# Performance work log

Measured on AMD Instinct MI355X. Metric: run time of the kernel, lower is better.

## Reference

```python
import jax, jax.numpy as jnp
import numpy as np
from jax import lax

LATENT = 64
NUM_EMB = 512
BETA = 0.25
DN = ('NCHW', 'OIHW', 'NCHW')


def conv(x, w, b, stride, pad):
    y = lax.conv_general_dilated(x, w, (stride, stride), [(pad, pad), (pad, pad)],
                                 dimension_numbers=DN)
    return y + b[None, :, None, None]


def tconv(x, w, b, stride, pad, opad):
    # torch ConvTranspose2d(k=3, stride, padding=pad, output_padding=opad)
    # == dilated conv with lhs_dilation=stride, padding (k-1-pad, k-1-pad+opad),
    #    spatially-flipped kernel. w is stored OIHW (out, in, kh, kw).
    k = w.shape[2]
    lo, hi = k - 1 - pad, k - 1 - pad + opad
    y = lax.conv_general_dilated(x, w[:, :, ::-1, ::-1], (1, 1), [(lo, hi), (lo, hi)],
                                 lhs_dilation=(stride, stride), dimension_numbers=DN)
    return y + b[None, :, None, None]


def vector_quantize(z, codebook):
    # z: (B, D, H, W); codebook: (K, D)
    B, D, H, W = z.shape
    flat = z.transpose(0, 2, 3, 1).reshape(-1, D)  # (BHW, D)
    d = (jnp.sum(flat ** 2, axis=1, keepdims=True)
         + jnp.sum(codebook ** 2, axis=1)
         - 2.0 * flat @ codebook.T)  # (BHW, K)
    idx = jnp.argmin(d, axis=1)
    q = codebook[idx].reshape(B, H, W, D).transpose(0, 3, 1, 2)  # (B, D, H, W)
    commitment = jnp.mean((lax.stop_gradient(q) - z) ** 2)
    codebook_loss = jnp.mean((q - lax.stop_gradient(z)) ** 2)
    loss = BETA * commitment + codebook_loss
    q_ste = z + lax.stop_gradient(q - z)  # straight-through estimator
    return q_ste, loss


def setup_inputs() -> dict:
    key = jax.random.key(0)
    ks = jax.random.split(key, 16)
    f32 = jnp.float32
    inp = {
        'x': jax.random.uniform(ks[0], (1024, 1, 50, 50), dtype=f32),
        'enc_w1': jax.random.normal(ks[1], (32, 1, 3, 3), f32) * 0.1,
        'enc_b1': jnp.zeros((32,), f32),
        'enc_w2': jax.random.normal(ks[2], (64, 32, 3, 3), f32) * 0.05,
        'enc_b2': jnp.zeros((64,), f32),
        'enc_w3': jax.random.normal(ks[3], (LATENT, 64, 1, 1), f32) * 0.1,
        'enc_b3': jnp.zeros((LATENT,), f32),
        'codebook': jax.random.uniform(ks[4], (NUM_EMB, LATENT), dtype=f32),
        'dec_w1': jax.random.normal(ks[5], (64, LATENT, 3, 3), f32) * 0.05,
        'dec_b1': jnp.zeros((64,), f32),
        'dec_w2': jax.random.normal(ks[6], (32, 64, 3, 3), f32) * 0.05,
        'dec_b2': jnp.zeros((32,), f32),
        'dec_w3': jax.random.normal(ks[7], (1, 32, 3, 3), f32) * 0.05,
        'dec_b3': jnp.zeros((1,), f32),
    }
    return inp


def reference(x, enc_w1, enc_b1, enc_w2, enc_b2, enc_w3, enc_b3, codebook,
              dec_w1, dec_b1, dec_w2, dec_b2, dec_w3, dec_b3):
    # encoder: (B,1,50,50) -> (B,LATENT,13,13)
    h = jax.nn.relu(conv(x, enc_w1, enc_b1, 2, 1))
    h = jax.nn.relu(conv(h, enc_w2, enc_b2, 2, 1))
    z = conv(h, enc_w3, enc_b3, 1, 0)
    q, vq_loss = vector_quantize(z, codebook)
    # decoder: 13 -> 25 -> 50
    h = jax.nn.relu(tconv(q, dec_w1, dec_b1, 2, 1, 0))
    h = jax.nn.relu(tconv(h, dec_w2, dec_b2, 2, 1, 1))
    x_recon = jax.nn.sigmoid(conv(h, dec_w3, dec_b3, 1, 1))
    return x_recon, vq_loss
```

## Files before the change

kernel.cpp:

```cpp
#include <hip/hip_runtime.h>
#include <math.h>


typedef __attribute__((ext_vector_type(8))) short s8v;
typedef __attribute__((ext_vector_type(4))) float f4v;
typedef __attribute__((ext_vector_type(4))) int i4v;

__device__ inline unsigned short f2bf(float f) {
    unsigned u = __builtin_bit_cast(unsigned, f);
    return (unsigned short)((u + 0x7fffu + ((u >> 16) & 1u)) >> 16);
}
__device__ inline float bf2f(unsigned short h) {
    return __builtin_bit_cast(float, ((unsigned)h) << 16);
}

__global__ __launch_bounds__(256) void k_prep_all(
        const float* __restrict__ cb,  const float* __restrict__ ew2,
        const float* __restrict__ ew3, const float* __restrict__ dw1,
        const float* __restrict__ dw2,
        unsigned short* __restrict__ cbm, unsigned short* __restrict__ wB2n,
        unsigned short* __restrict__ wB1, unsigned short* __restrict__ wB2,
        unsigned short* __restrict__ wB3, float* __restrict__ cn,
        float* __restrict__ loss) {
    int i = blockIdx.x * 256 + threadIdx.x;
    if (i < 98304) {
        int j = i & 7, lane = (i >> 3) & 63;
        int kc = (i >> 9) % 6, nt = (i >> 9) / 6;
        int n = nt * 16 + (lane & 15);
        int k = kc * 32 + ((lane >> 4) << 3) + j;
        int seg = k >> 6, kk = k & 63;
        float c = cb[n * 64 + kk];
        unsigned short ch = f2bf(c);
        cbm[i] = (seg == 1) ? f2bf(c - bf2f(ch)) : ch;
    } else if (i < 153600) {
        int q = i - 98304;
        int j = q & 7, lane = (q >> 3) & 63;
        int kc = (q >> 9) % 27, nt = (q >> 9) / 27;
        int k = kc * 32 + ((lane >> 4) << 3) + j;
        int co = nt * 16 + (lane & 15);
        int part = (k < 288) ? 0 : (k < 576) ? 1 : 0;
        int kk = (k < 288) ? k : (k < 576) ? k - 288 : k - 576;
        int tap = kk >> 5, ci = kk & 31;
        float v = ew2[(co * 32 + ci) * 9 + tap];
        unsigned short hi = f2bf(v);
        wB2n[q] = part ? f2bf(v - bf2f(hi)) : hi;
    } else if (i < 219136) {
        int q = i - 153600;
        int j = q & 7, l = (q >> 3) & 63, kc = (q >> 9) & 7, nt = q >> 12;
        int n = nt * 16 + (l & 15), k = kc * 32 + (l >> 4) * 8 + j;
        int cls = n >> 6, co = n & 63, p = k >> 6, ci = k & 63;
        int jh = -1, jw = -1;
        if (cls == 0)      { if (p == 0) { jh = 1; jw = 1; } }
        else if (cls == 1) { if (p == 1) { jh = 1; jw = 0; } else if (p == 0) { jh = 1; jw = 2; } }
        else if (cls == 2) { if (p == 2) { jh = 0; jw = 1; } else if (p == 0) { jh = 2; jw = 1; } }
        else { if (p == 3) { jh = 0; jw = 0; } else if (p == 2) { jh = 0; jw = 2; }
               else if (p == 1) { jh = 2; jw = 0; } else { jh = 2; jw = 2; } }
        float v = (jh >= 0) ? dw1[((co * 64 + ci) * 3 + jh) * 3 + jw] : 0.f;
        wB1[q] = f2bf(v);
    } else if (i < 251904) {
        int q = i - 219136;
        int j = q & 7, l = (q >> 3) & 63, kc = (q >> 9) & 7, nt = q >> 12;
        int n = nt * 16 + (l & 15), k = kc * 32 + (l >> 4) * 8 + j;
        int cls = n >> 5, co = n & 31, p = k >> 6, ci = k & 63;
        int jh = -1, jw = -1;
        if (cls == 0)      { if (p == 0) { jh = 1; jw = 1; } }
        else if (cls == 1) { if (p == 1) { jh = 1; jw = 0; } else if (p == 0) { jh = 1; jw = 2; } }
        else if (cls == 2) { if (p == 2) { jh = 0; jw = 1; } else if (p == 0) { jh = 2; jw = 1; } }
        else { if (p == 3) { jh = 0; jw = 0; } else if (p == 2) { jh = 0; jw = 2; }
               else if (p == 1) { jh = 2; jw = 0; } else { jh = 2; jw = 2; } }
        float v = (jh >= 0) ? dw2[((co * 64 + ci) * 3 + jh) * 3 + jw] : 0.f;
        wB2[q] = f2bf(v);
    } else if (i < 264192) {
        int q = i - 251904;
        int j = q & 7, lane = (q >> 3) & 63;
        int kc = (q >> 9) % 6, nt = (q >> 9) / 6;
        int k = kc * 32 + ((lane >> 4) << 3) + j;
        int n = nt * 16 + (lane & 15);
        int part = (k < 64) ? 0 : (k < 128) ? 1 : 0;
        int kk = (k < 64) ? k : (k < 128) ? k - 64 : k - 128;
        float v = ew3[n * 64 + kk];
        unsigned short hi = f2bf(v);
        wB3[q] = part ? f2bf(v - bf2f(hi)) : hi;
    } else if (i < 264704) {
        int k = i - 264192;
        const float* r = cb + k * 64;
        float s = 0.f;
#pragma unroll
        for (int c = 0; c < 64; ++c) s += r[c] * r[c];
        cn[k] = s;
    } else if (i == 264704) {
        *loss = 0.f;
    }
}

__global__ __launch_bounds__(256) void k_conv1(const float* __restrict__ x,
                                               const float* __restrict__ w,
                                               const float* __restrict__ b,
                                               float* __restrict__ h1, int total) {
    __shared__ float4 wl4[72];
    float* wl = (float*)wl4;
    int tid = threadIdx.x;
    for (int t = tid; t < 288; t += 256) {
        int tap = t >> 5, co = t & 31;
        wl[t] = w[co * 9 + tap];
    }
    __syncthreads();
    int pix = blockIdx.x * 256 + tid;
    if (pix >= total) return;
    int n = pix / 625, p = pix % 625, oh = p / 25, ow = p % 25;
    const float* xp = x + (size_t)n * 2500;
    float4 a[8];
#pragma unroll
    for (int j = 0; j < 8; ++j) a[j] = ((const float4*)b)[j];
#pragma unroll
    for (int kh = 0; kh < 3; ++kh) {
        int ih = 2 * oh - 1 + kh;
        if ((unsigned)ih >= 50u) continue;
#pragma unroll
        for (int kw = 0; kw < 3; ++kw) {
            int iw = 2 * ow - 1 + kw;
            if ((unsigned)iw >= 50u) continue;
            float v = xp[ih * 50 + iw];
            int tap = kh * 3 + kw;
#pragma unroll
            for (int j = 0; j < 8; ++j) {
                float4 ww = wl4[tap * 8 + j];
                a[j].x += v * ww.x; a[j].y += v * ww.y;
                a[j].z += v * ww.z; a[j].w += v * ww.w;
            }
        }
    }
    float4* op = (float4*)(h1 + (size_t)pix * 32);
#pragma unroll
    for (int j = 0; j < 8; ++j) {
        float4 r;
        r.x = fmaxf(a[j].x, 0.f); r.y = fmaxf(a[j].y, 0.f);
        r.z = fmaxf(a[j].z, 0.f); r.w = fmaxf(a[j].w, 0.f);
        op[j] = r;
    }
}

__global__ __launch_bounds__(256) void k_enc_m(const float* __restrict__ h1,
                                               const unsigned short* __restrict__ B2n,
                                               const unsigned short* __restrict__ B3,
                                               const float* __restrict__ b2,
                                               const float* __restrict__ b3,
                                               float* __restrict__ z, int npix) {
    __shared__ short a1[16 * 872];
    __shared__ short a2[16 * 200];
    __shared__ float cz[16 * 68];
    int tid = threadIdx.x, blk = blockIdx.x;
    {
        int m = tid >> 4, chunk = tid & 15;
        if (chunk < 9) {
            int pix = blk * 16 + m;
            float4 v[8];
            const float4 zero = {0.f, 0.f, 0.f, 0.f};
            bool ok = false;
            if (pix < npix) {
                int n = pix / 169, p = pix % 169, oh = p / 13, ow = p % 13;
                int kh = chunk / 3, kw = chunk % 3;
                int ih = 2 * oh - 1 + kh, iw = 2 * ow - 1 + kw;
                ok = ((unsigned)ih < 25u) && ((unsigned)iw < 25u);
                if (ok) {
                    const float4* ip = (const float4*)(h1 + (((size_t)n * 25 + ih) * 25 + iw) * 32);
#pragma unroll
                    for (int c4 = 0; c4 < 8; ++c4) v[c4] = ip[c4];
                }
            }
            if (!ok) {
#pragma unroll
                for (int c4 = 0; c4 < 8; ++c4) v[c4] = zero;
            }
            unsigned short hi[32], lo[32];
#pragma unroll
            for (int c4 = 0; c4 < 8; ++c4) {
                float vv[4] = {v[c4].x, v[c4].y, v[c4].z, v[c4].w};
#pragma unroll
                for (int e = 0; e < 4; ++e) {
                    int ci = c4 * 4 + e;
                    unsigned short h = f2bf(vv[e]);
                    hi[ci] = h;
                    lo[ci] = f2bf(vv[e] - bf2f(h));
                }
            }
            short* row = a1 + m * 872 + chunk * 32;
            i4v* d0 = (i4v*)row;
            i4v* d1 = (i4v*)(row + 288);
            i4v* d2 = (i4v*)(row + 576);
#pragma unroll
            for (int g = 0; g < 4; ++g) {
                i4v ph, pl;
#pragma unroll
                for (int e = 0; e < 4; ++e) {
                    int b0 = g * 8 + e * 2;
                    ph[e] = (int)((unsigned)hi[b0] | ((unsigned)hi[b0 + 1] << 16));
                    pl[e] = (int)((unsigned)lo[b0] | ((unsigned)lo[b0 + 1] << 16));
                }
                d0[g] = ph; d1[g] = ph; d2[g] = pl;
            }
        }
    }
    __syncthreads();
    int wave = tid >> 6, lane = tid & 63;
    int arow1 = (lane & 15) * 872 + (lane >> 4) * 8;
    f4v acc = (f4v){0.f, 0.f, 0.f, 0.f};
#pragma unroll
    for (int kc = 0; kc < 27; ++kc) {
        s8v a = *(const s8v*)(a1 + arow1 + kc * 32);
        s8v b = *(const s8v*)((const short*)B2n + ((size_t)((wave * 27 + kc) * 64 + lane)) * 8);
        acc = __builtin_amdgcn_mfma_f32_16x16x32_bf16(a, b, acc, 0, 0, 0);
    }
    {
        float bv = b2[wave * 16 + (lane & 15)];
        int n = wave * 16 + (lane & 15);
#pragma unroll
        for (int r = 0; r < 4; ++r) {
            int m = (lane >> 4) * 4 + r;
            float h = fmaxf(acc[r] + bv, 0.f);
            unsigned short hh = f2bf(h);
            unsigned short ll = f2bf(h - bf2f(hh));
            a2[m * 200 + n] = (short)hh;
            a2[m * 200 + 64 + n] = (short)hh;
            a2[m * 200 + 128 + n] = (short)ll;
        }
    }
    __syncthreads();
    int arow2 = (lane & 15) * 200 + (lane >> 4) * 8;
    f4v acc2 = (f4v){0.f, 0.f, 0.f, 0.f};
#pragma unroll
    for (int kc = 0; kc < 6; ++kc) {
        s8v a = *(const s8v*)(a2 + arow2 + kc * 32);
        s8v b = *(const s8v*)((const short*)B3 + ((size_t)((wave * 6 + kc) * 64 + lane)) * 8);
        acc2 = __builtin_amdgcn_mfma_f32_16x16x32_bf16(a, b, acc2, 0, 0, 0);
    }
    {
        float bv = b3[wave * 16 + (lane & 15)];
        int n = wave * 16 + (lane & 15);
#pragma unroll
        for (int r = 0; r < 4; ++r) {
            int m = (lane >> 4) * 4 + r;
            cz[m * 68 + n] = acc2[r] + bv;
        }
    }
    __syncthreads();
    {
        int m = tid >> 4, c4 = tid & 15;
        int pix = blk * 16 + m;
        if (pix < npix) {
            float4 v = *(float4*)(cz + m * 68 + c4 * 4);
            *(float4*)(z + (size_t)pix * 64 + c4 * 4) = v;
        }
    }
}

__global__ __launch_bounds__(256) void k_vq_m(const float* __restrict__ z,
                                              const float* __restrict__ cb,
                                              const unsigned short* __restrict__ cbm,
                                              const float* __restrict__ cn,
                                              float* __restrict__ q,
                                              float* __restrict__ loss, int npix) {
    __shared__ short a_lds[64 * 200];
    __shared__ float reds[4 * 64];
    __shared__ int   redk[4 * 64];
    __shared__ int   bkf[64];
    __shared__ float lred[4];
    int tid = threadIdx.x, blk = blockIdx.x;
#pragma unroll
    for (int it = 0; it < 2; ++it) {
        int idx = tid + it * 256;
        int m = idx >> 3, p = idx & 7;
        int pix = blk * 64 + m;
        unsigned short zh[8], zl[8];
        if (pix < npix) {
            const float* src = z + (size_t)pix * 64 + p * 8;
#pragma unroll
            for (int v = 0; v < 8; ++v) {
                float f = src[v];
                unsigned short h = f2bf(f);
                zh[v] = h; zl[v] = f2bf(f - bf2f(h));
            }
        } else {
#pragma unroll
            for (int v = 0; v < 8; ++v) { zh[v] = 0; zl[v] = 0; }
        }
        unsigned ph[4], pl[4];
#pragma unroll
        for (int v = 0; v < 4; ++v) {
            ph[v] = (unsigned)zh[2 * v] | ((unsigned)zh[2 * v + 1] << 16);
            pl[v] = (unsigned)zl[2 * v] | ((unsigned)zl[2 * v + 1] << 16);
        }
        short* row = a_lds + m * 200;
        i4v vh = (i4v){(int)ph[0], (int)ph[1], (int)ph[2], (int)ph[3]};
        i4v vl = (i4v){(int)pl[0], (int)pl[1], (int)pl[2], (int)pl[3]};
        *(i4v*)(row + p * 8) = vh;
        *(i4v*)(row + 64 + p * 8) = vh;
        *(i4v*)(row + 128 + p * 8) = vl;
    }
    __syncthreads();
    int wave = tid >> 6, lane = tid & 63;
    s8v af[4][6];
#pragma unroll
    for (int mt = 0; mt < 4; ++mt) {
        int arow = (mt * 16 + (lane & 15)) * 200 + (lane >> 4) * 8;
#pragma unroll
        for (int kc = 0; kc < 6; ++kc)
            af[mt][kc] = *(const s8v*)(a_lds + arow + kc * 32);
    }
    float bd[4][4];
    int bk[4][4];
#pragma unroll
    for (int mt = 0; mt < 4; ++mt)
#pragma unroll
        for (int r = 0; r < 4; ++r) { bd[mt][r] = 3.4e38f; bk[mt][r] = 0; }
#pragma unroll 1
    for (int nt = 0; nt < 8; ++nt) {
        int ntg = wave * 8 + nt;
        s8v bf[6];
#pragma unroll
        for (int kc = 0; kc < 6; ++kc)
            bf[kc] = *(const s8v*)((const short*)cbm + ((size_t)((ntg * 6 + kc) * 64 + lane)) * 8);
        f4v acc[4];
#pragma unroll
        for (int mt = 0; mt < 4; ++mt) acc[mt] = (f4v){0.f, 0.f, 0.f, 0.f};
#pragma unroll
        for (int kc = 0; kc < 6; ++kc) {
#pragma unroll
            for (int mt = 0; mt < 4; ++mt)
                acc[mt] = __builtin_amdgcn_mfma_f32_16x16x32_bf16(af[mt][kc], bf[kc], acc[mt], 0, 0, 0);
        }
        int kcol = ntg * 16 + (lane & 15);
        float cnk = cn[kcol];
#pragma unroll
        for (int mt = 0; mt < 4; ++mt)
#pragma unroll
            for (int r = 0; r < 4; ++r) {
                float d = cnk - 2.f * acc[mt][r];
                if (d < bd[mt][r]) { bd[mt][r] = d; bk[mt][r] = kcol; }
            }
    }
#pragma unroll
    for (int off = 1; off < 16; off <<= 1) {
#pragma unroll
        for (int mt = 0; mt < 4; ++mt)
#pragma unroll
            for (int r = 0; r < 4; ++r) {
                float od = __shfl_xor(bd[mt][r], off);
                int ok = __shfl_xor(bk[mt][r], off);
                if (od < bd[mt][r] || (od == bd[mt][r] && ok < bk[mt][r])) {
                    bd[mt][r] = od; bk[mt][r] = ok;
                }
            }
    }
    if ((lane & 15) == 0) {
#pragma unroll
        for (int mt = 0; mt < 4; ++mt)
#pragma unroll
            for (int r = 0; r < 4; ++r) {
                int m = mt * 16 + (lane >> 4) * 4 + r;
                reds[wave * 64 + m] = bd[mt][r];
                redk[wave * 64 + m] = bk[mt][r];
            }
    }
    __syncthreads();
    if (tid < 64) {
        float d0 = reds[tid]; int k0 = redk[tid];
#pragma unroll
        for (int w = 1; w < 4; ++w) {
            float dw = reds[w * 64 + tid]; int kw = redk[w * 64 + tid];
            if (dw < d0 || (dw == d0 && kw < k0)) { d0 = dw; k0 = kw; }
        }
        bkf[tid] = k0;
    }
    __syncthreads();
    float lsum = 0.f;
#pragma unroll
    for (int it = 0; it < 4; ++it) {
        int idx = tid + it * 256;
        int m = idx >> 4, c4 = idx & 15;
        int pix = blk * 64 + m;
        if (pix < npix) {
            int k0 = bkf[m];
            float4 cq = ((const float4*)cb)[(size_t)k0 * 16 + c4];
            float4 zz = ((const float4*)(z + (size_t)pix * 64))[c4];
            float dx = cq.x - zz.x, dy = cq.y - zz.y, dz = cq.z - zz.z, dw = cq.w - zz.w;
            lsum += dx * dx + dy * dy + dz * dz + dw * dw;
            ((float4*)(q + (size_t)pix * 64))[c4] = cq;
        }
    }
#pragma unroll
    for (int off = 32; off > 0; off >>= 1) lsum += __shfl_down(lsum, off);
    if ((tid & 63) == 0) lred[tid >> 6] = lsum;
    __syncthreads();
    if (tid == 0) {
        float t = lred[0] + lred[1] + lred[2] + lred[3];
        atomicAdd(loss, t * (1.25f / 11075584.f));
    }
}

__global__ __launch_bounds__(256) void k_tconv1_m(const float* __restrict__ q,
                                                  const unsigned short* __restrict__ wB,
                                                  const float* __restrict__ bias,
                                                  unsigned short* __restrict__ d1,
                                                  int nquad) {
    __shared__ short a_lds[32 * 264];
    __shared__ short c_lds[32 * 264];
    int tid = threadIdx.x, blk = blockIdx.x;
#pragma unroll
    for (int pass = 0; pass < 4; ++pass) {
        int idx = tid + pass * 256;
        int m = idx >> 5, sub = idx & 31;
        int qg = blk * 32 + m;
        int p = sub >> 3, ci0 = (sub & 7) * 8;
        unsigned short t8[8];
        bool have = false;
        if (qg < nquad) {
            int img = qg / 169, r = qg % 169, qm = r / 13, qw = r % 13;
            int sm = qm + (p >> 1), sw = qw + (p & 1);
            if (sm < 13 && sw < 13) {
                const float* src = q + (((size_t)img * 13 + sm) * 13 + sw) * 64 + ci0;
#pragma unroll
                for (int v = 0; v < 8; ++v) t8[v] = f2bf(src[v]);
                have = true;
            }
        }
        if (!have) {
#pragma unroll
            for (int v = 0; v < 8; ++v) t8[v] = 0;
        }
        i4v pk;
#pragma unroll
        for (int e = 0; e < 4; ++e)
            pk[e] = (int)((unsigned)t8[2 * e] | ((unsigned)t8[2 * e + 1] << 16));
        *(i4v*)(a_lds + m * 264 + sub * 8) = pk;
    }
    __syncthreads();
    int wave = tid >> 6, lane = tid & 63;
    f4v acc[2][4];
#pragma unroll
    for (int mt = 0; mt < 2; ++mt)
#pragma unroll
        for (int i = 0; i < 4; ++i) acc[mt][i] = (f4v){0.f, 0.f, 0.f, 0.f};
    float bv[4];
#pragma unroll
    for (int i = 0; i < 4; ++i) bv[i] = bias[((wave * 4 + i) * 16 + (lane & 15)) & 63];
#pragma unroll
    for (int kc = 0; kc < 8; ++kc) {
        s8v a0 = *(const s8v*)(a_lds + ((lane & 15)) * 264 + (lane >> 4) * 8 + kc * 32);
        s8v a1 = *(const s8v*)(a_lds + (16 + (lane & 15)) * 264 + (lane >> 4) * 8 + kc * 32);
#pragma unroll
        for (int i = 0; i < 4; ++i) {
            int nt = wave * 4 + i;
            s8v b = *(const s8v*)((const short*)wB + ((size_t)((nt * 8 + kc) * 64 + lane)) * 8);
            acc[0][i] = __builtin_amdgcn_mfma_f32_16x16x32_bf16(a0, b, acc[0][i], 0, 0, 0);
            acc[1][i] = __builtin_amdgcn_mfma_f32_16x16x32_bf16(a1, b, acc[1][i], 0, 0, 0);
        }
    }
#pragma unroll
    for (int mt = 0; mt < 2; ++mt)
#pragma unroll
        for (int i = 0; i < 4; ++i) {
            int n = (wave * 4 + i) * 16 + (lane & 15);
#pragma unroll
            for (int r2 = 0; r2 < 4; ++r2) {
                int m = mt * 16 + (lane >> 4) * 4 + r2;
                float v = fmaxf(acc[mt][i][r2] + bv[i], 0.f);
                c_lds[m * 264 + n] = (short)f2bf(v);
            }
        }
    __syncthreads();
#pragma unroll
    for (int pass = 0; pass < 4; ++pass) {
        int ch = tid + pass * 256;
        int m = ch >> 5, cpart = ch & 31;
        int qg = blk * 32 + m;
        if (qg >= nquad) continue;
        int img = qg / 169, r = qg % 169, qm = r / 13, qw = r % 13;
        int cls = cpart >> 3, co8 = (cpart & 7) * 8;
        int oh = 2 * qm + (cls >> 1), ow = 2 * qw + (cls & 1);
        if (oh >= 25 || ow >= 25) continue;
        i4v val = *(i4v*)(c_lds + m * 264 + cls * 64 + co8);
        *(i4v*)(d1 + (((size_t)img * 25 + oh) * 25 + ow) * 64 + co8) = val;
    }
}

__global__ __launch_bounds__(256) void k_tconv2_m(const unsigned short* __restrict__ d1,
                                                  const unsigned short* __restrict__ wB,
                                                  const float* __restrict__ bias,
                                                  unsigned short* __restrict__ d2,
                                                  int nquad) {
    __shared__ short a_lds[32 * 264];
    __shared__ short c_lds[32 * 136];
    int tid = threadIdx.x, blk = blockIdx.x;
#pragma unroll
    for (int pass = 0; pass < 4; ++pass) {
        int idx = tid + pass * 256;
        int m = idx >> 5, sub = idx & 31;
        int qg = blk * 32 + m;
        int p = sub >> 3, ci0 = (sub & 7) * 8;
        i4v v = (i4v){0, 0, 0, 0};
        if (qg < nquad) {
            int img = qg / 625, r = qg % 625, qm = r / 25, qw = r % 25;
            int sm = qm + (p >> 1), sw = qw + (p & 1);
            if (sm < 25 && sw < 25)
                v = *(const i4v*)(d1 + (((size_t)img * 25 + sm) * 25 + sw) * 64 + ci0);
        }
        *(i4v*)(a_lds + m * 264 + sub * 8) = v;
    }
    __syncthreads();
    int wave = tid >> 6, lane = tid & 63;
    f4v acc[2][2];
#pragma unroll
    for (int mt = 0; mt < 2; ++mt)
#pragma unroll
        for (int i = 0; i < 2; ++i) acc[mt][i] = (f4v){0.f, 0.f, 0.f, 0.f};
    float bv[2];
#pragma unroll
    for (int i = 0; i < 2; ++i) bv[i] = bias[((wave * 2 + i) * 16 + (lane & 15)) & 31];
#pragma unroll
    for (int kc = 0; kc < 8; ++kc) {
        s8v a0 = *(const s8v*)(a_lds + ((lane & 15)) * 264 + (lane >> 4) * 8 + kc * 32);
        s8v a1 = *(const s8v*)(a_lds + (16 + (lane & 15)) * 264 + (lane >> 4) * 8 + kc * 32);
#pragma unroll
        for (int i = 0; i < 2; ++i) {
            int nt = wave * 2 + i;
            s8v b = *(const s8v*)((const short*)wB + ((size_t)((nt * 8 + kc) * 64 + lane)) * 8);
            acc[0][i] = __builtin_amdgcn_mfma_f32_16x16x32_bf16(a0, b, acc[0][i], 0, 0, 0);
            acc[1][i] = __builtin_amdgcn_mfma_f32_16x16x32_bf16(a1, b, acc[1][i], 0, 0, 0);
        }
    }
#pragma unroll
    for (int mt = 0; mt < 2; ++mt)
#pragma unroll
        for (int i = 0; i < 2; ++i) {
            int n = (wave * 2 + i) * 16 + (lane & 15);
#pragma unroll
            for (int r2 = 0; r2 < 4; ++r2) {
                int m = mt * 16 + (lane >> 4) * 4 + r2;
                float v = fmaxf(acc[mt][i][r2] + bv[i], 0.f);
                c_lds[m * 136 + n] = (short)f2bf(v);
            }
        }
    __syncthreads();
#pragma unroll
    for (int pass = 0; pass < 2; ++pass) {
        int ch = tid + pass * 256;
        int m = ch >> 4, cpart = ch & 15;
        int qg = blk * 32 + m;
        if (qg >= nquad) continue;
        int img = qg / 625, r = qg % 625, qm = r / 25, qw = r % 25;
        int cls = cpart >> 2, co8 = (cpart & 3) * 8;
        int oh = 2 * qm + (cls >> 1), ow = 2 * qw + (cls & 1);
        i4v val = *(i4v*)(c_lds + m * 136 + cls * 32 + co8);
        *(i4v*)(d2 + (((size_t)img * 50 + oh) * 50 + ow) * 32 + co8) = val;
    }
}

__global__ __launch_bounds__(256) void k_convf(const unsigned short* __restrict__ in,
                                               const float* __restrict__ w,
                                               const float* __restrict__ b,
                                               float* __restrict__ out, int total) {
    __shared__ float wl[288];
    int tid = threadIdx.x;
    for (int t = tid; t < 288; t += 256) {
        int tap = t >> 5, ci = t & 31;
        wl[t] = w[ci * 9 + tap];
    }
    __syncthreads();
    int pix = blockIdx.x * 256 + tid;
    if (pix >= total) return;
    int n = pix / 2500, p = pix % 2500, oh = p / 50, ow = p % 50;
    float acc = b[0];
#pragma unroll
    for (int kh = 0; kh < 3; ++kh) {
        int ih = oh - 1 + kh;
        if ((unsigned)ih >= 50u) continue;
#pragma unroll
        for (int kw = 0; kw < 3; ++kw) {
            int iw = ow - 1 + kw;
            if ((unsigned)iw >= 50u) continue;
            const float* wt = wl + (kh * 3 + kw) * 32;
            const i4v* ip4 = (const i4v*)(in + (((size_t)n * 50 + ih) * 50 + iw) * 32);
#pragma unroll
            for (int c8 = 0; c8 < 4; ++c8) {
                i4v u = ip4[c8];
#pragma unroll
                for (int e = 0; e < 4; ++e) {
                    unsigned uu = (unsigned)u[e];
                    float x0 = __builtin_bit_cast(float, uu << 16);
                    float x1 = __builtin_bit_cast(float, uu & 0xffff0000u);
                    acc = fmaf(x0, wt[c8 * 8 + e * 2], acc);
                    acc = fmaf(x1, wt[c8 * 8 + e * 2 + 1], acc);
                }
            }
        }
    }
    out[pix] = 1.f / (1.f + expf(-acc));
}

extern "C" void kernel_launch(void* const* d_in, const int* in_sizes, int n_in,
                              void* d_out, int out_size, void* d_ws, size_t ws_size,
                              hipStream_t stream) {
    const float* x   = (const float*)d_in[0];
    const float* ew1 = (const float*)d_in[1];
    const float* eb1 = (const float*)d_in[2];
    const float* ew2 = (const float*)d_in[3];
    const float* eb2 = (const float*)d_in[4];
    const float* ew3 = (const float*)d_in[5];
    const float* eb3 = (const float*)d_in[6];
    const float* cb  = (const float*)d_in[7];
    const float* dw1 = (const float*)d_in[8];
    const float* db1 = (const float*)d_in[9];
    const float* dw2 = (const float*)d_in[10];
    const float* db2 = (const float*)d_in[11];
    const float* dw3 = (const float*)d_in[12];
    const float* db3 = (const float*)d_in[13];
    float* out = (float*)d_out;
    float* loss = out + 2560000;

    float* ws = (float*)d_ws;
    float* cn = ws;
    unsigned short* wB1  = (unsigned short*)(ws + 512);
    unsigned short* wB2  = (unsigned short*)(ws + 33280);
    unsigned short* wB2n = (unsigned short*)(ws + 49664);
    unsigned short* wB3  = (unsigned short*)(ws + 77312);
    unsigned short* cbm  = (unsigned short*)(ws + 83456);
    const size_t tw_floats = 132608;

    const int B = 1024;
    const size_t A_per = 40000, B_per = 20000;
    size_t avail = (ws_size / 4 > tw_floats) ? ws_size / 4 - tw_floats : 0;
    int BC = (int)(avail / (A_per + B_per));
    if (BC > B) BC = B;
    if (BC < 1) BC = 1;
    float* regA = ws + tw_floats;
    float* regB = regA + (size_t)BC * A_per;

    k_prep_all<<<1035, 256, 0, stream>>>(cb, ew2, ew3, dw1, dw2,
                                         cbm, wB2n, wB1, wB2, wB3, cn, loss);

    for (int n0 = 0; n0 < B; n0 += BC) {
        int bc = (B - n0 < BC) ? (B - n0) : BC;
        const float* xch = x + (size_t)n0 * 2500;

        int t1 = bc * 625;
        k_conv1<<<(t1 + 255) / 256, 256, 0, stream>>>(xch, ew1, eb1, regA, t1);

        int npix = bc * 169;
        k_enc_m<<<(npix + 15) / 16, 256, 0, stream>>>(regA, wB2n, wB3, eb2, eb3, regB, npix);

        k_vq_m<<<(npix + 63) / 64, 256, 0, stream>>>(regB, cb, cbm, cn, regA, loss, npix);

        unsigned short* d1 = (unsigned short*)regB;
        k_tconv1_m<<<(npix + 31) / 32, 256, 0, stream>>>(regA, wB1, db1, d1, npix);

        int nq2 = bc * 625;
        unsigned short* d2 = (unsigned short*)regA;
        k_tconv2_m<<<(nq2 + 31) / 32, 256, 0, stream>>>(d1, wB2, db2, d2, nq2);

        int t6 = bc * 2500;
        k_convf<<<(t6 + 255) / 256, 256, 0, stream>>>(d2, dw3, db3, out + (size_t)n0 * 2500, t6);
    }
}
```

Measured before the change: 503.7 us.

## Retile encoder and VQ kernels to 32-pixel blocks and dedupe hi LDS copies

The encoder MFMA kernel now handles 32 pixels per block with two M-tiles, so each B fragment loaded from global memory is reused twice. It also stops writing the duplicated bf16 'hi' copy to LDS and indexes the hi part twice instead, which shrinks LDS footprint and store traffic. The VQ kernel goes the other way, from 64 to 32 pixels per block, doubling grid size for occupancy, and unrolls its codebook loop by 2. In exchange, the VQ kernel loads each codebook fragment half as many times per pixel tile, so codebook reads roughly double.

Result: no change. 506.4 us (+0.5%).

```diff
diff --git a/kernel.cpp b/kernel.cpp
--- a/kernel.cpp
+++ b/kernel.cpp
@@ -146,14 +146,16 @@
                                                const float* __restrict__ b2,
                                                const float* __restrict__ b3,
                                                float* __restrict__ z, int npix) {
-    __shared__ short a1[16 * 872];
-    __shared__ short a2[16 * 200];
-    __shared__ float cz[16 * 68];
+    __shared__ short a1[32 * 584];
+    __shared__ short a2[32 * 136];
+    __shared__ float cz[32 * 68];
     int tid = threadIdx.x, blk = blockIdx.x;
-    {
-        int m = tid >> 4, chunk = tid & 15;
-        if (chunk < 9) {
-            int pix = blk * 16 + m;
+#pragma unroll
+    for (int it = 0; it < 2; ++it) {
+        int idx = tid + it * 256;
+        if (idx < 288) {
+            int m = idx / 9, chunk = idx % 9;
+            int pix = blk * 32 + m;
             float4 v[8];
             const float4 zero = {0.f, 0.f, 0.f, 0.f};
             bool ok = false;
@@ -184,10 +186,9 @@
                     lo[ci] = f2bf(vv[e] - bf2f(h));
                 }
             }
-            short* row = a1 + m * 872 + chunk * 32;
-            i4v* d0 = (i4v*)row;
-            i4v* d1 = (i4v*)(row + 288);
-            i4v* d2 = (i4v*)(row + 576);
+            short* row = a1 + m * 584;
+            i4v* dh = (i4v*)(row + chunk * 32);
+            i4v* dl = (i4v*)(row + 288 + chunk * 32);
 #pragma unroll
             for (int g = 0; g < 4; ++g) {
                 i4v ph, pl;
@@ -197,56 +198,72 @@
                     ph[e] = (int)((unsigned)hi[b0] | ((unsigned)hi[b0 + 1] << 16));
                     pl[e] = (int)((unsigned)lo[b0] | ((unsigned)lo[b0 + 1] << 16));
                 }
-                d0[g] = ph; d1[g] = ph; d2[g] = pl;
+                dh[g] = ph; dl[g] = pl;
             }
         }
     }
     __syncthreads();
     int wave = tid >> 6, lane = tid & 63;
-    int arow1 = (lane & 15) * 872 + (lane >> 4) * 8;
-    f4v acc = (f4v){0.f, 0.f, 0.f, 0.f};
+    int acol = (lane >> 4) * 8;
+    f4v acc[2];
+    acc[0] = (f4v){0.f, 0.f, 0.f, 0.f};
+    acc[1] = acc[0];
 #pragma unroll
     for (int kc = 0; kc < 27; ++kc) {
-        s8v a = *(const s8v*)(a1 + arow1 + kc * 32);
+        int aoff = (kc < 9) ? kc * 32 : (kc < 18) ? (kc - 9) * 32 : 288 + (kc - 18) * 32;
         s8v b = *(const s8v*)((const short*)B2n + ((size_t)((wave * 27 + kc) * 64 + lane)) * 8);
-        acc = __builtin_amdgcn_mfma_f32_16x16x32_bf16(a, b, acc, 0, 0, 0);
+#pragma unroll
+        for (int mt = 0; mt < 2; ++mt) {
+            s8v a = *(const s8v*)(a1 + (mt * 16 + (lane & 15)) * 584 + acol + aoff);
+            acc[mt] = __builtin_amdgcn_mfma_f32_16x16x32_bf16(a, b, acc[mt], 0, 0, 0);
+        }
     }
     {
         float bv = b2[wave * 16 + (lane & 15)];
         int n = wave * 16 + (lane & 15);
 #pragma unroll
-        for (int r = 0; r < 4; ++r) {
-            int m = (lane >> 4) * 4 + r;
-            float h = fmaxf(acc[r] + bv, 0.f);
-            unsigned short hh = f2bf(h);
-            unsigned short ll = f2bf(h - bf2f(hh));
-            a2[m * 200 + n] = (short)hh;
-            a2[m * 200 + 64 + n] = (short)hh;
-            a2[m * 200 + 128 + n] = (short)ll;
-        }
-    }
-    __syncthreads();
-    int arow2 = (lane & 15) * 200 + (lane >> 4) * 8;
-    f4v acc2 = (f4v){0.f, 0.f, 0.f, 0.f};
+        for (int mt = 0; mt < 2; ++mt)
+#pragma unroll
+            for (int r = 0; r < 4; ++r) {
+                int m = mt * 16 + (lane >> 4) * 4 + r;
+                float h = fmaxf(acc[mt][r] + bv, 0.f);
+                unsigned short hh = f2bf(h);
+                unsigned short ll = f2bf(h - bf2f(hh));
+                a2[m * 136 + n] = (short)hh;
+                a2[m * 136 + 64 + n] = (short)ll;
+            }
+    }
+    __syncthreads();
+    f4v acc2[2];
+    acc2[0] = (f4v){0.f, 0.f, 0.f, 0.f};
+    acc2[1] = acc2[0];
 #pragma unroll
     for (int kc = 0; kc < 6; ++kc) {
-        s8v a = *(const s8v*)(a2 + arow2 + kc * 32);
+        int aoff = (kc < 2) ? kc * 32 : (kc < 4) ? (kc - 2) * 32 : 64 + (kc - 4) * 32;
         s8v b = *(const s8v*)((const short*)B3 + ((size_t)((wave * 6 + kc) * 64 + lane)) * 8);
-        acc2 = __builtin_amdgcn_mfma_f32_16x16x32_bf16(a, b, acc2, 0, 0, 0);
+#pragma unroll
+        for (int mt = 0; mt < 2; ++mt) {
+            s8v a = *(const s8v*)(a2 + (mt * 16 + (lane & 15)) * 136 + acol + aoff);
+            acc2[mt] = __builtin_amdgcn_mfma_f32_16x16x32_bf16(a, b, acc2[mt], 0, 0, 0);
+        }
     }
     {
         float bv = b3[wave * 16 + (lane & 15)];
         int n = wave * 16 + (lane & 15);
 #pragma unroll
-        for (int r = 0; r < 4; ++r) {
-            int m = (lane >> 4) * 4 + r;
-            cz[m * 68 + n] = acc2[r] + bv;
-        }
-    }
-    __syncthreads();
-    {
-        int m = tid >> 4, c4 = tid & 15;
-        int pix = blk * 16 + m;
+        for (int mt = 0; mt < 2; ++mt)
+#pragma unroll
+            for (int r = 0; r < 4; ++r) {
+                int m = mt * 16 + (lane >> 4) * 4 + r;
+                cz[m * 68 + n] = acc2[mt][r] + bv;
+            }
+    }
+    __syncthreads();
+#pragma unroll
+    for (int it = 0; it < 2; ++it) {
+        int idx = tid + it * 256;
+        int m = idx >> 4, c4 = idx & 15;
+        int pix = blk * 32 + m;
         if (pix < npix) {
             float4 v = *(float4*)(cz + m * 68 + c4 * 4);
             *(float4*)(z + (size_t)pix * 64 + c4 * 4) = v;
@@ -260,17 +277,15 @@
                                               const float* __restrict__ cn,
                                               float* __restrict__ q,
                                               float* __restrict__ loss, int npix) {
-    __shared__ short a_lds[64 * 200];
-    __shared__ float reds[4 * 64];
-    __shared__ int   redk[4 * 64];
-    __shared__ int   bkf[64];
+    __shared__ short a_lds[32 * 200];
+    __shared__ float reds[4 * 32];
+    __shared__ int   redk[4 * 32];
+    __shared__ int   bkf[32];
     __shared__ float lred[4];
     int tid = threadIdx.x, blk = blockIdx.x;
-#pragma unroll
-    for (int it = 0; it < 2; ++it) {
-        int idx = tid + it * 256;
-        int m = idx >> 3, p = idx & 7;
-        int pix = blk * 64 + m;
+    {
+        int m = tid >> 3, p = tid & 7;
+        int pix = blk * 32 + m;
         unsigned short zh[8], zl[8];
         if (pix < npix) {
             const float* src = z + (size_t)pix * 64 + p * 8;
@@ -299,50 +314,48 @@
     }
     __syncthreads();
     int wave = tid >> 6, lane = tid & 63;
-    s8v af[4][6];
-#pragma unroll
-    for (int mt = 0; mt < 4; ++mt) {
+    s8v af[2][6];
+#pragma unroll
+    for (int mt = 0; mt < 2; ++mt) {
         int arow = (mt * 16 + (lane & 15)) * 200 + (lane >> 4) * 8;
 #pragma unroll
         for (int kc = 0; kc < 6; ++kc)
             af[mt][kc] = *(const s8v*)(a_lds + arow + kc * 32);
     }
-    float bd[4][4];
-    int bk[4][4];
-#pragma unroll
-    for (int mt = 0; mt < 4; ++mt)
+    float bd[2][4];
+    int bk[2][4];
+#pragma unroll
+    for (int mt = 0; mt < 2; ++mt)
 #pragma unroll
         for (int r = 0; r < 4; ++r) { bd[mt][r] = 3.4e38f; bk[mt][r] = 0; }
-#pragma unroll 1
+#pragma unroll 2
     for (int nt = 0; nt < 8; ++nt) {
         int ntg = wave * 8 + nt;
         s8v bf[6];
 #pragma unroll
         for (int kc = 0; kc < 6; ++kc)
             bf[kc] = *(const s8v*)((const short*)cbm + ((size_t)((ntg * 6 + kc) * 64 + lane)) * 8);
-        f4v acc[4];
-#pragma unroll
-        for (int mt = 0; mt < 4; ++mt) acc[mt] = (f4v){0.f, 0.f, 0.f, 0.f};
+        f4v acc0 = (f4v){0.f, 0.f, 0.f, 0.f};
+        f4v acc1 = (f4v){0.f, 0.f, 0.f, 0.f};
 #pragma unroll
         for (int kc = 0; kc < 6; ++kc) {
-#pragma unroll
-            for (int mt = 0; mt < 4; ++mt)
-                acc[mt] = __builtin_amdgcn_mfma_f32_16x16x32_bf16(af[mt][kc], bf[kc], acc[mt], 0, 0, 0);
+            acc0 = __builtin_amdgcn_mfma_f32_16x16x32_bf16(af[0][kc], bf[kc], acc0, 0, 0, 0);
+            acc1 = __builtin_amdgcn_mfma_f32_16x16x32_bf16(af[1][kc], bf[kc], acc1, 0, 0, 0);
         }
         int kcol = ntg * 16 + (lane & 15);
         float cnk = cn[kcol];
 #pragma unroll
-        for (int mt = 0; mt < 4; ++mt)
-#pragma unroll
-            for (int r = 0; r < 4; ++r) {
-                float d = cnk - 2.f * acc[mt][r];
-                if (d < bd[mt][r]) { bd[mt][r] = d; bk[mt][r] = kcol; }
-            }
+        for (int r = 0; r < 4; ++r) {
+            float d0 = cnk - 2.f * acc0[r];
+            if (d0 < bd[0][r]) { bd[0][r] = d0; bk[0][r] = kcol; }
+            float d1 = cnk - 2.f * acc1[r];
+            if (d1 < bd[1][r]) { bd[1][r] = d1; bk[1][r] = kcol; }
+        }
     }
 #pragma unroll
     for (int off = 1; off < 16; off <<= 1) {
 #pragma unroll
-        for (int mt = 0; mt < 4; ++mt)
+        for (int mt = 0; mt < 2; ++mt)
 #pragma unroll
             for (int r = 0; r < 4; ++r) {
                 float od = __shfl_xor(bd[mt][r], off);
@@ -354,20 +367,20 @@
     }
     if ((lane & 15) == 0) {
 #pragma unroll
-        for (int mt = 0; mt < 4; ++mt)
+        for (int mt = 0; mt < 2; ++mt)
 #pragma unroll
             for (int r = 0; r < 4; ++r) {
                 int m = mt * 16 + (lane >> 4) * 4 + r;
-                reds[wave * 64 + m] = bd[mt][r];
-                redk[wave * 64 + m] = bk[mt][r];
-            }
-    }
-    __syncthreads();
-    if (tid < 64) {
+                reds[wave * 32 + m] = bd[mt][r];
+                redk[wave * 32 + m] = bk[mt][r];
+            }
+    }
+    __syncthreads();
+    if (tid < 32) {
         float d0 = reds[tid]; int k0 = redk[tid];
 #pragma unroll
         for (int w = 1; w < 4; ++w) {
-            float dw = reds[w * 64 + tid]; int kw = redk[w * 64 + tid];
+            float dw = reds[w * 32 + tid]; int kw = redk[w * 32 + tid];
             if (dw < d0 || (dw == d0 && kw < k0)) { d0 = dw; k0 = kw; }
         }
         bkf[tid] = k0;
@@ -375,10 +388,9 @@
     __syncthreads();
     float lsum = 0.f;
 #pragma unroll
-    for (int it = 0; it < 4; ++it) {
-        int idx = tid + it * 256;
-        int m = idx >> 4, c4 = idx & 15;
-        int pix = blk * 64 + m;
+    for (int it = 0; it < 2; ++it) {
+        int m = tid >> 3, c4 = (tid & 7) + it * 8;
+        int pix = blk * 32 + m;
         if (pix < npix) {
             int k0 = bkf[m];
             float4 cq = ((const float4*)cb)[(size_t)k0 * 16 + c4];
@@ -647,9 +659,9 @@
         k_conv1<<<(t1 + 255) / 256, 256, 0, stream>>>(xch, ew1, eb1, regA, t1);
 
         int npix = bc * 169;
-        k_enc_m<<<(npix + 15) / 16, 256, 0, stream>>>(regA, wB2n, wB3, eb2, eb3, regB, npix);
-
-        k_vq_m<<<(npix + 63) / 64, 256, 0, stream>>>(regB, cb, cbm, cn, regA, loss, npix);
+        k_enc_m<<<(npix + 31) / 32, 256, 0, stream>>>(regA, wB2n, wB3, eb2, eb3, regB, npix);
+
+        k_vq_m<<<(npix + 31) / 32, 256, 0, stream>>>(regB, cb, cbm, cn, regA, loss, npix);
 
         unsigned short* d1 = (unsigned short*)regB;
         k_tconv1_m<<<(npix + 31) / 32, 256, 0, stream>>>(regA, wB1, db1, d1, npix);
```
